# Kernel tuning notes

Hardware: AMD Instinct MI355X
Metric: run time of the kernel (lower is better)

## Reference

```python
import jax, jax.numpy as jnp
import numpy as np

L, B, D, N = 4096, 4, 1024, 16


def setup_inputs() -> dict:
    key = jax.random.key(0)
    ks = jax.random.split(key, 6)
    x = jax.random.normal(ks[0], (L, B, D), dtype=jnp.float32)
    delta = 0.2 * jax.random.normal(ks[1], (D, N, 1), dtype=jnp.float32)
    alpha = 0.2 * jax.random.normal(ks[2], (D, N, 1), dtype=jnp.float32)
    # beta init: N(0, 0.02) + 1.0 (val is all ones since i % 1 == 0 always)
    beta = 0.02 * jax.random.normal(ks[3], (D, N, 1), dtype=jnp.float32) + 1.0
    gamma = jax.random.normal(ks[4], (D, N), dtype=jnp.float32)
    omega = jax.random.normal(ks[5], (D,), dtype=jnp.float32)
    return {"x": x, "delta": delta, "alpha": alpha, "beta": beta,
            "gamma": gamma, "omega": omega}


def reference(x, delta, alpha, beta, gamma, omega):
    seq_len = x.shape[0]
    scale = (1.0 / gamma.shape[1]) ** 0.5
    # EMA coefficients
    p = jax.nn.sigmoid(delta)                      # (D, N, 1)
    q = 1.0 - p * jax.nn.sigmoid(alpha)            # (D, N, 1)
    # Vandermonde kernel: k[d, l] = sum_n p*beta * q^l * gamma*scale
    t = jnp.arange(seq_len, dtype=x.dtype)         # (L,)
    vander = t[None, None, :] * jnp.log(q)         # (D, N, L)
    kernel = p * beta * jnp.exp(vander)            # (D, N, L)
    k = jnp.einsum('dnl,dn->dl', kernel, gamma * scale)  # (D, L)
    # Residual path
    residual = x * omega                           # (L, B, D)
    # FFT causal convolution along time
    xt = jnp.transpose(x, (1, 2, 0))               # (B, D, L)
    n_fft = 2 * seq_len
    k_f = jnp.fft.rfft(k.astype(jnp.float32), n=n_fft)      # (D, n_fft//2+1)
    x_f = jnp.fft.rfft(xt.astype(jnp.float32), n=n_fft)     # (B, D, n_fft//2+1)
    out = jnp.fft.irfft(x_f * k_f, n=n_fft)[..., :seq_len]  # (B, D, L)
    out = out.astype(x.dtype)
    out = jax.nn.silu(jnp.transpose(out, (2, 0, 1)) + residual)  # (L, B, D)
    return out
```

## Files before the change

### kernel.cpp

```cpp
#include <hip/hip_runtime.h>
#include <hip/hip_cooperative_groups.h>
#include <math.h>

namespace cg = cooperative_groups;

#define D_SZ 1024
#define N_MODES 16
#define CH 4096
#define ROW 4096
#define C_CHUNKS 64
#define LC 64

__device__ __forceinline__ void load16(const float* __restrict__ p, int d, float v[16]) {
    const float4* p4 = (const float4*)(p + (size_t)d * 16);
#pragma unroll
    for (int r = 0; r < 4; ++r) {
        float4 t = p4[r];
        v[4*r+0] = t.x; v[4*r+1] = t.y; v[4*r+2] = t.z; v[4*r+3] = t.w;
    }
}

__device__ __forceinline__ void compute_qw(const float* __restrict__ delta,
                                           const float* __restrict__ alpha,
                                           const float* __restrict__ beta,
                                           const float* __restrict__ gamma,
                                           int d, float q[16], float w[16]) {
    float dl[16], al[16], bt[16], gm[16];
    load16(delta, d, dl); load16(alpha, d, al);
    load16(beta, d, bt);  load16(gamma, d, gm);
#pragma unroll
    for (int n = 0; n < 16; ++n) {
        float p  = 1.0f / (1.0f + __expf(-dl[n]));
        float sa = 1.0f / (1.0f + __expf(-al[n]));
        q[n] = 1.0f - p * sa;
        w[n] = p * bt[n] * gm[n] * 0.25f;
    }
}

__device__ __forceinline__ void phase1_body(const float* __restrict__ x, float* __restrict__ S,
    const float* __restrict__ delta, const float* __restrict__ alpha,
    const float* __restrict__ beta, const float* __restrict__ gamma, int j, int c) {
    int d = c & (D_SZ - 1);
    float q[16], w[16];
    compute_qw(delta, alpha, beta, gamma, d, q, w);
    float h[16];
#pragma unroll
    for (int n = 0; n < 16; ++n) h[n] = 0.0f;
    const float* xp = x + (size_t)j * (LC * ROW) + c;
#pragma unroll 2
    for (int s0 = 0; s0 < LC; s0 += 8) {
        float xv[8];
#pragma unroll
        for (int u = 0; u < 8; ++u) xv[u] = xp[(size_t)(s0 + u) * ROW];
#pragma unroll
        for (int u = 0; u < 8; ++u)
#pragma unroll
            for (int n = 0; n < 16; ++n) h[n] = fmaf(q[n], h[n], xv[u]);
    }
    float4* Sp = (float4*)(S + ((size_t)j * CH + c) * 16);
#pragma unroll
    for (int r = 0; r < 4; ++r)
        Sp[r] = make_float4(h[4*r], h[4*r+1], h[4*r+2], h[4*r+3]);
}

__device__ __forceinline__ void phase2_body(float* __restrict__ S,
    const float* __restrict__ delta, const float* __restrict__ alpha, int c2, int lane) {
    int d = c2 & (D_SZ - 1);
    float dl[16], al[16];
    load16(delta, d, dl); load16(alpha, d, al);
    float pw[16];
#pragma unroll
    for (int n = 0; n < 16; ++n) {
        float p  = 1.0f / (1.0f + __expf(-dl[n]));
        float sa = 1.0f / (1.0f + __expf(-al[n]));
        float qn = 1.0f - p * sa;
#pragma unroll
        for (int t = 0; t < 6; ++t) qn *= qn;
        pw[n] = qn;
    }
    float hh[16];
    float4* Sp = (float4*)(S + ((size_t)lane * CH + c2) * 16);
#pragma unroll
    for (int r = 0; r < 4; ++r) {
        float4 t = Sp[r];
        hh[4*r] = t.x; hh[4*r+1] = t.y; hh[4*r+2] = t.z; hh[4*r+3] = t.w;
    }
#pragma unroll
    for (int k = 1; k <= 32; k <<= 1) {
        float prev[16];
#pragma unroll
        for (int n = 0; n < 16; ++n) prev[n] = __shfl_up(hh[n], (unsigned)k, 64);
#pragma unroll
        for (int n = 0; n < 16; ++n) hh[n] = (lane >= k) ? fmaf(pw[n], prev[n], hh[n]) : hh[n];
#pragma unroll
        for (int n = 0; n < 16; ++n) pw[n] *= pw[n];
    }
    float cin[16];
#pragma unroll
    for (int n = 0; n < 16; ++n) {
        float t = __shfl_up(hh[n], 1u, 64);
        cin[n] = (lane == 0) ? 0.0f : t;
    }
#pragma unroll
    for (int r = 0; r < 4; ++r)
        Sp[r] = make_float4(cin[4*r], cin[4*r+1], cin[4*r+2], cin[4*r+3]);
}

__device__ __forceinline__ void phase3_body(const float* __restrict__ x,
    const float* __restrict__ S, float* __restrict__ out,
    const float* __restrict__ delta, const float* __restrict__ alpha,
    const float* __restrict__ beta, const float* __restrict__ gamma,
    const float* __restrict__ omega, int j, int c) {
    int d = c & (D_SZ - 1);
    float q[16], w[16];
    compute_qw(delta, alpha, beta, gamma, d, q, w);
    float om = omega[d];
    float h[16];
    const float4* Sp = (const float4*)(S + ((size_t)j * CH + c) * 16);
#pragma unroll
    for (int r = 0; r < 4; ++r) {
        float4 t = Sp[r];
        h[4*r] = t.x; h[4*r+1] = t.y; h[4*r+2] = t.z; h[4*r+3] = t.w;
    }
    size_t base = (size_t)j * (LC * ROW) + c;
#pragma unroll 2
    for (int s0 = 0; s0 < LC; s0 += 8) {
        float xv[8];
#pragma unroll
        for (int u = 0; u < 8; ++u) xv[u] = x[base + (size_t)(s0 + u) * ROW];
#pragma unroll
        for (int u = 0; u < 8; ++u) {
            float xu = xv[u];
            float y0 = 0.0f, y1 = 0.0f, y2 = 0.0f, y3 = 0.0f;
#pragma unroll
            for (int n = 0; n < 16; n += 4) {
                h[n]   = fmaf(q[n],   h[n],   xu); y0 = fmaf(w[n],   h[n],   y0);
                h[n+1] = fmaf(q[n+1], h[n+1], xu); y1 = fmaf(w[n+1], h[n+1], y1);
                h[n+2] = fmaf(q[n+2], h[n+2], xu); y2 = fmaf(w[n+2], h[n+2], y2);
                h[n+3] = fmaf(q[n+3], h[n+3], xu); y3 = fmaf(w[n+3], h[n+3], y3);
            }
            float z = (y0 + y1) + (y2 + y3) + xu * om;
            float r = z / (1.0f + __expf(-z));
            __builtin_nontemporal_store(r, &out[base + (size_t)(s0 + u) * ROW]);
        }
    }
}

__global__ __launch_bounds__(256, 4) void ema_fused(
    const float* __restrict__ x, const float* __restrict__ delta,
    const float* __restrict__ alpha, const float* __restrict__ beta,
    const float* __restrict__ gamma, const float* __restrict__ omega,
    float* __restrict__ S, float* __restrict__ out) {
    int tid = threadIdx.x;
    int j = blockIdx.x;
    int c = blockIdx.y * 256 + tid;
    phase1_body(x, S, delta, alpha, beta, gamma, j, c);
    cg::this_grid().sync();
    int gb = blockIdx.y * gridDim.x + blockIdx.x;
    phase2_body(S, delta, alpha, gb * 4 + (tid >> 6), tid & 63);
    cg::this_grid().sync();
    phase3_body(x, S, out, delta, alpha, beta, gamma, omega, j, c);
}

__global__ __launch_bounds__(256) void k_phase1(const float* __restrict__ x, float* __restrict__ S,
    const float* __restrict__ delta, const float* __restrict__ alpha,
    const float* __restrict__ beta, const float* __restrict__ gamma) {
    phase1_body(x, S, delta, alpha, beta, gamma, blockIdx.x, blockIdx.y * 256 + threadIdx.x);
}
__global__ __launch_bounds__(256) void k_phase2(float* __restrict__ S,
    const float* __restrict__ delta, const float* __restrict__ alpha) {
    phase2_body(S, delta, alpha, blockIdx.x * 4 + (threadIdx.x >> 6), threadIdx.x & 63);
}
__global__ __launch_bounds__(256) void k_phase3(const float* __restrict__ x,
    const float* __restrict__ S, float* __restrict__ out,
    const float* __restrict__ delta, const float* __restrict__ alpha,
    const float* __restrict__ beta, const float* __restrict__ gamma,
    const float* __restrict__ omega) {
    phase3_body(x, S, out, delta, alpha, beta, gamma, omega,
                blockIdx.x, blockIdx.y * 256 + threadIdx.x);
}

extern "C" void kernel_launch(void* const* d_in, const int* in_sizes, int n_in,
                              void* d_out, int out_size, void* d_ws, size_t ws_size,
                              hipStream_t stream) {
    const float* x     = (const float*)d_in[0];
    const float* delta = (const float*)d_in[1];
    const float* alpha = (const float*)d_in[2];
    const float* beta  = (const float*)d_in[3];
    const float* gamma = (const float*)d_in[4];
    const float* omega = (const float*)d_in[5];
    float* out = (float*)d_out;
    float* S   = (float*)d_ws;

    dim3 grid(C_CHUNKS, CH / 256);

    int maxBlocks = 0;
    hipError_t e = hipOccupancyMaxActiveBlocksPerMultiprocessor(
        &maxBlocks, (const void*)ema_fused, 256, 0);
    if (e == hipSuccess && maxBlocks >= 4) {
        void* args[] = {(void*)&x, (void*)&delta, (void*)&alpha, (void*)&beta,
                        (void*)&gamma, (void*)&omega, (void*)&S, (void*)&out};
        hipLaunchCooperativeKernel((const void*)ema_fused, grid, dim3(256, 1, 1),
                                   args, 0, stream);
    } else {
        k_phase1<<<grid, 256, 0, stream>>>(x, S, delta, alpha, beta, gamma);
        k_phase2<<<CH / 4, 256, 0, stream>>>(S, delta, alpha);
        k_phase3<<<grid, 256, 0, stream>>>(x, S, out, delta, alpha, beta, gamma, omega);
    }
}
```

Before: 164.5 us.

## Double-buffer x tiles through LDS with float4 loads in scan phases

Phases 1 and 3 now stage x through shared memory in 16-row sub-tiles using float4 global loads, double-buffered so the next sub-tile's loads are issued while the current one is consumed from LDS. This aims to replace scalar strided loads with wider coalesced loads and to hide global memory latency behind the recurrence FMAs. The cost is 32 KB of LDS per block plus extra __syncthreads, which may lower occupancy and break the cooperative-launch requirement of 4 blocks per CU, causing a fallback to the three-kernel path.

```diff
diff --git a/kernel.cpp b/kernel.cpp
--- a/kernel.cpp
+++ b/kernel.cpp
@@ -5,11 +5,13 @@
 namespace cg = cooperative_groups;
 
 #define D_SZ 1024
-#define N_MODES 16
 #define CH 4096
 #define ROW 4096
 #define C_CHUNKS 64
 #define LC 64
+#define SUB 16
+#define NSUB (LC / SUB)
+#define TILE_F (SUB * 256)
 
 __device__ __forceinline__ void load16(const float* __restrict__ p, int d, float v[16]) {
     const float4* p4 = (const float4*)(p + (size_t)d * 16);
@@ -37,30 +39,53 @@
     }
 }
 
+__device__ __forceinline__ void stage_issue(const float* __restrict__ x,
+                                            size_t rowBase, int tid, float4 r[4]) {
+    const float* p = x + rowBase + (size_t)(tid >> 6) * ROW + ((tid & 63) << 2);
+#pragma unroll
+    for (int k = 0; k < 4; ++k)
+        r[k] = *(const float4*)(p + (size_t)(4 * k) * ROW);
+}
+
+__device__ __forceinline__ void stage_commit(float* __restrict__ buf, int tid,
+                                             const float4 r[4]) {
+#pragma unroll
+    for (int k = 0; k < 4; ++k)
+        *(float4*)(buf + ((tid >> 6) + 4 * k) * 256 + ((tid & 63) << 2)) = r[k];
+}
+
 __device__ __forceinline__ void phase1_body(const float* __restrict__ x, float* __restrict__ S,
     const float* __restrict__ delta, const float* __restrict__ alpha,
-    const float* __restrict__ beta, const float* __restrict__ gamma, int j, int c) {
+    const float* __restrict__ beta, const float* __restrict__ gamma,
+    int j, int cgrp, int tid, float* __restrict__ lds) {
+    int c = cgrp * 256 + tid;
     int d = c & (D_SZ - 1);
     float q[16], w[16];
     compute_qw(delta, alpha, beta, gamma, d, q, w);
     float h[16];
 #pragma unroll
     for (int n = 0; n < 16; ++n) h[n] = 0.0f;
-    const float* xp = x + (size_t)j * (LC * ROW) + c;
-#pragma unroll 2
-    for (int s0 = 0; s0 < LC; s0 += 8) {
-        float xv[8];
-#pragma unroll
-        for (int u = 0; u < 8; ++u) xv[u] = xp[(size_t)(s0 + u) * ROW];
-#pragma unroll
-        for (int u = 0; u < 8; ++u)
-#pragma unroll
-            for (int n = 0; n < 16; ++n) h[n] = fmaf(q[n], h[n], xv[u]);
+
+    size_t rb = (size_t)(j * LC) * ROW + (size_t)cgrp * 256;
+    float4 r[4];
+    stage_issue(x, rb, tid, r);
+    stage_commit(lds, tid, r);
+    for (int st = 0; st < NSUB; ++st) {
+        if (st + 1 < NSUB) stage_issue(x, rb + (size_t)((st + 1) * SUB) * ROW, tid, r);
+        __syncthreads();
+        const float* cb = lds + (st & 1) * TILE_F;
+#pragma unroll
+        for (int l = 0; l < SUB; ++l) {
+            float xu = cb[l * 256 + tid];
+#pragma unroll
+            for (int n = 0; n < 16; ++n) h[n] = fmaf(q[n], h[n], xu);
+        }
+        if (st + 1 < NSUB) stage_commit(lds + ((st + 1) & 1) * TILE_F, tid, r);
     }
     float4* Sp = (float4*)(S + ((size_t)j * CH + c) * 16);
 #pragma unroll
-    for (int r = 0; r < 4; ++r)
-        Sp[r] = make_float4(h[4*r], h[4*r+1], h[4*r+2], h[4*r+3]);
+    for (int rr = 0; rr < 4; ++rr)
+        Sp[rr] = make_float4(h[4*rr], h[4*rr+1], h[4*rr+2], h[4*rr+3]);
 }
 
 __device__ __forceinline__ void phase2_body(float* __restrict__ S,
@@ -81,9 +106,9 @@
     float hh[16];
     float4* Sp = (float4*)(S + ((size_t)lane * CH + c2) * 16);
 #pragma unroll
-    for (int r = 0; r < 4; ++r) {
-        float4 t = Sp[r];
-        hh[4*r] = t.x; hh[4*r+1] = t.y; hh[4*r+2] = t.z; hh[4*r+3] = t.w;
+    for (int rr = 0; rr < 4; ++rr) {
+        float4 t = Sp[rr];
+        hh[4*rr] = t.x; hh[4*rr+1] = t.y; hh[4*rr+2] = t.z; hh[4*rr+3] = t.w;
     }
 #pragma unroll
     for (int k = 1; k <= 32; k <<= 1) {
@@ -102,15 +127,16 @@
         cin[n] = (lane == 0) ? 0.0f : t;
     }
 #pragma unroll
-    for (int r = 0; r < 4; ++r)
-        Sp[r] = make_float4(cin[4*r], cin[4*r+1], cin[4*r+2], cin[4*r+3]);
+    for (int rr = 0; rr < 4; ++rr)
+        Sp[rr] = make_float4(cin[4*rr], cin[4*rr+1], cin[4*rr+2], cin[4*rr+3]);
 }
 
 __device__ __forceinline__ void phase3_body(const float* __restrict__ x,
     const float* __restrict__ S, float* __restrict__ out,
     const float* __restrict__ delta, const float* __restrict__ alpha,
     const float* __restrict__ beta, const float* __restrict__ gamma,
-    const float* __restrict__ omega, int j, int c) {
+    const float* __restrict__ omega, int j, int cgrp, int tid, float* __restrict__ lds) {
+    int c = cgrp * 256 + tid;
     int d = c & (D_SZ - 1);
     float q[16], w[16];
     compute_qw(delta, alpha, beta, gamma, d, q, w);
@@ -118,19 +144,23 @@
     float h[16];
     const float4* Sp = (const float4*)(S + ((size_t)j * CH + c) * 16);
 #pragma unroll
-    for (int r = 0; r < 4; ++r) {
-        float4 t = Sp[r];
-        h[4*r] = t.x; h[4*r+1] = t.y; h[4*r+2] = t.z; h[4*r+3] = t.w;
-    }
-    size_t base = (size_t)j * (LC * ROW) + c;
-#pragma unroll 2
-    for (int s0 = 0; s0 < LC; s0 += 8) {
-        float xv[8];
-#pragma unroll
-        for (int u = 0; u < 8; ++u) xv[u] = x[base + (size_t)(s0 + u) * ROW];
-#pragma unroll
-        for (int u = 0; u < 8; ++u) {
-            float xu = xv[u];
+    for (int rr = 0; rr < 4; ++rr) {
+        float4 t = Sp[rr];
+        h[4*rr] = t.x; h[4*rr+1] = t.y; h[4*rr+2] = t.z; h[4*rr+3] = t.w;
+    }
+
+    size_t rb = (size_t)(j * LC) * ROW + (size_t)cgrp * 256;
+    float4 r[4];
+    stage_issue(x, rb, tid, r);
+    stage_commit(lds, tid, r);
+    for (int st = 0; st < NSUB; ++st) {
+        if (st + 1 < NSUB) stage_issue(x, rb + (size_t)((st + 1) * SUB) * ROW, tid, r);
+        __syncthreads();
+        const float* cb = lds + (st & 1) * TILE_F;
+        size_t obase = rb + (size_t)(st * SUB) * ROW + (size_t)tid;
+#pragma unroll
+        for (int l = 0; l < SUB; ++l) {
+            float xu = cb[l * 256 + tid];
             float y0 = 0.0f, y1 = 0.0f, y2 = 0.0f, y3 = 0.0f;
 #pragma unroll
             for (int n = 0; n < 16; n += 4) {
@@ -140,9 +170,10 @@
                 h[n+3] = fmaf(q[n+3], h[n+3], xu); y3 = fmaf(w[n+3], h[n+3], y3);
             }
             float z = (y0 + y1) + (y2 + y3) + xu * om;
-            float r = z / (1.0f + __expf(-z));
-            __builtin_nontemporal_store(r, &out[base + (size_t)(s0 + u) * ROW]);
+            float res = z / (1.0f + __expf(-z));
+            __builtin_nontemporal_store(res, &out[obase + (size_t)l * ROW]);
         }
+        if (st + 1 < NSUB) stage_commit(lds + ((st + 1) & 1) * TILE_F, tid, r);
     }
 }
 
@@ -151,21 +182,23 @@
     const float* __restrict__ alpha, const float* __restrict__ beta,
     const float* __restrict__ gamma, const float* __restrict__ omega,
     float* __restrict__ S, float* __restrict__ out) {
+    __shared__ float lds[2 * TILE_F];
     int tid = threadIdx.x;
     int j = blockIdx.x;
-    int c = blockIdx.y * 256 + tid;
-    phase1_body(x, S, delta, alpha, beta, gamma, j, c);
+    int cgrp = blockIdx.y;
+    phase1_body(x, S, delta, alpha, beta, gamma, j, cgrp, tid, lds);
     cg::this_grid().sync();
-    int gb = blockIdx.y * gridDim.x + blockIdx.x;
+    int gb = cgrp * gridDim.x + j;
     phase2_body(S, delta, alpha, gb * 4 + (tid >> 6), tid & 63);
     cg::this_grid().sync();
-    phase3_body(x, S, out, delta, alpha, beta, gamma, omega, j, c);
+    phase3_body(x, S, out, delta, alpha, beta, gamma, omega, j, cgrp, tid, lds);
 }
 
 __global__ __launch_bounds__(256) void k_phase1(const float* __restrict__ x, float* __restrict__ S,
     const float* __restrict__ delta, const float* __restrict__ alpha,
     const float* __restrict__ beta, const float* __restrict__ gamma) {
-    phase1_body(x, S, delta, alpha, beta, gamma, blockIdx.x, blockIdx.y * 256 + threadIdx.x);
+    __shared__ float lds[2 * TILE_F];
+    phase1_body(x, S, delta, alpha, beta, gamma, blockIdx.x, blockIdx.y, threadIdx.x, lds);
 }
 __global__ __launch_bounds__(256) void k_phase2(float* __restrict__ S,
     const float* __restrict__ delta, const float* __restrict__ alpha) {
@@ -176,8 +209,9 @@
     const float* __restrict__ delta, const float* __restrict__ alpha,
     const float* __restrict__ beta, const float* __restrict__ gamma,
     const float* __restrict__ omega) {
+    __shared__ float lds[2 * TILE_F];
     phase3_body(x, S, out, delta, alpha, beta, gamma, omega,
-                blockIdx.x, blockIdx.y * 256 + threadIdx.x);
+                blockIdx.x, blockIdx.y, threadIdx.x, lds);
 }
 
 extern "C" void kernel_launch(void* const* d_in, const int* in_sizes, int n_in,
```

Measured after the change: 191.5 us. 1.16x slower.

## Replace cooperative fused kernel with three launches using 128 smaller chunks

Applied to the files above, without the earlier changes.

Drops the cooperative-groups fused kernel with grid syncs and always runs three separate kernels. The chunk count doubles to 128 with 32 timesteps each, and phase 2 handles two chunks per lane: it combines pairs serially before the 64-lane shuffle scan, then expands the result back. Phases 1 and 3 use explicit double-buffered register loads of x. Non-temporal output stores are removed. This trades grid-sync cost and the occupancy limit of the cooperative launch for extra launch overhead and doubled S workspace traffic.

```diff
diff --git a/kernel.cpp b/kernel.cpp
--- a/kernel.cpp
+++ b/kernel.cpp
@@ -1,15 +1,12 @@
 #include <hip/hip_runtime.h>
-#include <hip/hip_cooperative_groups.h>
 #include <math.h>
 
-namespace cg = cooperative_groups;
-
 #define D_SZ 1024
-#define N_MODES 16
 #define CH 4096
 #define ROW 4096
-#define C_CHUNKS 64
-#define LC 64
+#define C_CHUNKS 128
+#define LC 32
+#define SQ_LC 5
 
 __device__ __forceinline__ void load16(const float* __restrict__ p, int d, float v[16]) {
     const float4* p4 = (const float4*)(p + (size_t)d * 16);
@@ -37,54 +34,77 @@
     }
 }
 
-__device__ __forceinline__ void phase1_body(const float* __restrict__ x, float* __restrict__ S,
+__device__ __forceinline__ void loadg(const float* __restrict__ xp, int g, float v[8]) {
+#pragma unroll
+    for (int u = 0; u < 8; ++u) v[u] = xp[(size_t)(g * 8 + u) * ROW];
+}
+
+__device__ __forceinline__ void compg(float h[16], const float q[16], const float v[8]) {
+#pragma unroll
+    for (int u = 0; u < 8; ++u) {
+        float xu = v[u];
+#pragma unroll
+        for (int n = 0; n < 16; ++n) h[n] = fmaf(q[n], h[n], xu);
+    }
+}
+
+__global__ __launch_bounds__(256) void k_phase1(const float* __restrict__ x,
+    float* __restrict__ S,
     const float* __restrict__ delta, const float* __restrict__ alpha,
-    const float* __restrict__ beta, const float* __restrict__ gamma, int j, int c) {
+    const float* __restrict__ beta, const float* __restrict__ gamma) {
+    int tid = threadIdx.x;
+    int j = blockIdx.x;
+    int c = blockIdx.y * 256 + tid;
     int d = c & (D_SZ - 1);
     float q[16], w[16];
     compute_qw(delta, alpha, beta, gamma, d, q, w);
     float h[16];
 #pragma unroll
     for (int n = 0; n < 16; ++n) h[n] = 0.0f;
-    const float* xp = x + (size_t)j * (LC * ROW) + c;
-#pragma unroll 2
-    for (int s0 = 0; s0 < LC; s0 += 8) {
-        float xv[8];
-#pragma unroll
-        for (int u = 0; u < 8; ++u) xv[u] = xp[(size_t)(s0 + u) * ROW];
-#pragma unroll
-        for (int u = 0; u < 8; ++u)
-#pragma unroll
-            for (int n = 0; n < 16; ++n) h[n] = fmaf(q[n], h[n], xv[u]);
-    }
+    const float* xp = x + (size_t)j * LC * ROW + c;
+    float xa[8], xb[8];
+    loadg(xp, 0, xa);
+    loadg(xp, 1, xb); compg(h, q, xa);
+    loadg(xp, 2, xa); compg(h, q, xb);
+    loadg(xp, 3, xb); compg(h, q, xa);
+    compg(h, q, xb);
     float4* Sp = (float4*)(S + ((size_t)j * CH + c) * 16);
 #pragma unroll
     for (int r = 0; r < 4; ++r)
         Sp[r] = make_float4(h[4*r], h[4*r+1], h[4*r+2], h[4*r+3]);
 }
 
-__device__ __forceinline__ void phase2_body(float* __restrict__ S,
-    const float* __restrict__ delta, const float* __restrict__ alpha, int c2, int lane) {
-    int d = c2 & (D_SZ - 1);
+__global__ __launch_bounds__(256) void k_phase2(float* __restrict__ S,
+    const float* __restrict__ delta, const float* __restrict__ alpha) {
+    int lane = threadIdx.x & 63;
+    int wv   = threadIdx.x >> 6;
+    int c    = blockIdx.x * 4 + wv;
+    int d    = c & (D_SZ - 1);
     float dl[16], al[16];
     load16(delta, d, dl); load16(alpha, d, al);
-    float pw[16];
+    float A[16], pw[16];
 #pragma unroll
     for (int n = 0; n < 16; ++n) {
         float p  = 1.0f / (1.0f + __expf(-dl[n]));
         float sa = 1.0f / (1.0f + __expf(-al[n]));
         float qn = 1.0f - p * sa;
 #pragma unroll
-        for (int t = 0; t < 6; ++t) qn *= qn;
-        pw[n] = qn;
+        for (int t = 0; t < SQ_LC; ++t) qn *= qn;
+        A[n]  = qn;
+        pw[n] = qn * qn;
+    }
+    float4* Spa = (float4*)(S + ((size_t)(2 * lane)     * CH + c) * 16);
+    float4* Spb = (float4*)(S + ((size_t)(2 * lane + 1) * CH + c) * 16);
+    float sa16[16], sb16[16];
+#pragma unroll
+    for (int r = 0; r < 4; ++r) {
+        float4 ta = Spa[r], tb = Spb[r];
+        sa16[4*r] = ta.x; sa16[4*r+1] = ta.y; sa16[4*r+2] = ta.z; sa16[4*r+3] = ta.w;
+        sb16[4*r] = tb.x; sb16[4*r+1] = tb.y; sb16[4*r+2] = tb.z; sb16[4*r+3] = tb.w;
     }
     float hh[16];
-    float4* Sp = (float4*)(S + ((size_t)lane * CH + c2) * 16);
 #pragma unroll
-    for (int r = 0; r < 4; ++r) {
-        float4 t = Sp[r];
-        hh[4*r] = t.x; hh[4*r+1] = t.y; hh[4*r+2] = t.z; hh[4*r+3] = t.w;
-    }
+    for (int n = 0; n < 16; ++n) hh[n] = fmaf(A[n], sa16[n], sb16[n]);
 #pragma unroll
     for (int k = 1; k <= 32; k <<= 1) {
         float prev[16];
@@ -95,22 +115,49 @@
 #pragma unroll
         for (int n = 0; n < 16; ++n) pw[n] *= pw[n];
     }
-    float cin[16];
+    float Hb[16];
 #pragma unroll
     for (int n = 0; n < 16; ++n) {
         float t = __shfl_up(hh[n], 1u, 64);
-        cin[n] = (lane == 0) ? 0.0f : t;
+        Hb[n] = (lane == 0) ? 0.0f : t;
     }
 #pragma unroll
-    for (int r = 0; r < 4; ++r)
-        Sp[r] = make_float4(cin[4*r], cin[4*r+1], cin[4*r+2], cin[4*r+3]);
+    for (int r = 0; r < 4; ++r) {
+        Spa[r] = make_float4(Hb[4*r], Hb[4*r+1], Hb[4*r+2], Hb[4*r+3]);
+        Spb[r] = make_float4(fmaf(A[4*r],   Hb[4*r],   sa16[4*r]),
+                             fmaf(A[4*r+1], Hb[4*r+1], sa16[4*r+1]),
+                             fmaf(A[4*r+2], Hb[4*r+2], sa16[4*r+2]),
+                             fmaf(A[4*r+3], Hb[4*r+3], sa16[4*r+3]));
+    }
 }
 
-__device__ __forceinline__ void phase3_body(const float* __restrict__ x,
+__device__ __forceinline__ void comp_store(float h[16], const float q[16], const float w[16],
+                                           float om, const float v[8],
+                                           float* __restrict__ outp, int g) {
+#pragma unroll
+    for (int u = 0; u < 8; ++u) {
+        float xu = v[u];
+        float y0 = 0.0f, y1 = 0.0f, y2 = 0.0f, y3 = 0.0f;
+#pragma unroll
+        for (int n = 0; n < 16; n += 4) {
+            h[n]   = fmaf(q[n],   h[n],   xu); y0 = fmaf(w[n],   h[n],   y0);
+            h[n+1] = fmaf(q[n+1], h[n+1], xu); y1 = fmaf(w[n+1], h[n+1], y1);
+            h[n+2] = fmaf(q[n+2], h[n+2], xu); y2 = fmaf(w[n+2], h[n+2], y2);
+            h[n+3] = fmaf(q[n+3], h[n+3], xu); y3 = fmaf(w[n+3], h[n+3], y3);
+        }
+        float z = (y0 + y1) + (y2 + y3) + xu * om;
+        outp[(size_t)(g * 8 + u) * ROW] = z / (1.0f + __expf(-z));
+    }
+}
+
+__global__ __launch_bounds__(256) void k_phase3(const float* __restrict__ x,
     const float* __restrict__ S, float* __restrict__ out,
     const float* __restrict__ delta, const float* __restrict__ alpha,
     const float* __restrict__ beta, const float* __restrict__ gamma,
-    const float* __restrict__ omega, int j, int c) {
+    const float* __restrict__ omega) {
+    int tid = threadIdx.x;
+    int j = blockIdx.x;
+    int c = blockIdx.y * 256 + tid;
     int d = c & (D_SZ - 1);
     float q[16], w[16];
     compute_qw(delta, alpha, beta, gamma, d, q, w);
@@ -122,62 +169,14 @@
         float4 t = Sp[r];
         h[4*r] = t.x; h[4*r+1] = t.y; h[4*r+2] = t.z; h[4*r+3] = t.w;
     }
-    size_t base = (size_t)j * (LC * ROW) + c;
-#pragma unroll 2
-    for (int s0 = 0; s0 < LC; s0 += 8) {
-        float xv[8];
-#pragma unroll
-        for (int u = 0; u < 8; ++u) xv[u] = x[base + (size_t)(s0 + u) * ROW];
-#pragma unroll
-        for (int u = 0; u < 8; ++u) {
-            float xu = xv[u];
-            float y0 = 0.0f, y1 = 0.0f, y2 = 0.0f, y3 = 0.0f;
-#pragma unroll
-            for (int n = 0; n < 16; n += 4) {
-                h[n]   = fmaf(q[n],   h[n],   xu); y0 = fmaf(w[n],   h[n],   y0);
-                h[n+1] = fmaf(q[n+1], h[n+1], xu); y1 = fmaf(w[n+1], h[n+1], y1);
-                h[n+2] = fmaf(q[n+2], h[n+2], xu); y2 = fmaf(w[n+2], h[n+2], y2);
-                h[n+3] = fmaf(q[n+3], h[n+3], xu); y3 = fmaf(w[n+3], h[n+3], y3);
-            }
-            float z = (y0 + y1) + (y2 + y3) + xu * om;
-            float r = z / (1.0f + __expf(-z));
-            __builtin_nontemporal_store(r, &out[base + (size_t)(s0 + u) * ROW]);
-        }
-    }
-}
-
-__global__ __launch_bounds__(256, 4) void ema_fused(
-    const float* __restrict__ x, const float* __restrict__ delta,
-    const float* __restrict__ alpha, const float* __restrict__ beta,
-    const float* __restrict__ gamma, const float* __restrict__ omega,
-    float* __restrict__ S, float* __restrict__ out) {
-    int tid = threadIdx.x;
-    int j = blockIdx.x;
-    int c = blockIdx.y * 256 + tid;
-    phase1_body(x, S, delta, alpha, beta, gamma, j, c);
-    cg::this_grid().sync();
-    int gb = blockIdx.y * gridDim.x + blockIdx.x;
-    phase2_body(S, delta, alpha, gb * 4 + (tid >> 6), tid & 63);
-    cg::this_grid().sync();
-    phase3_body(x, S, out, delta, alpha, beta, gamma, omega, j, c);
-}
-
-__global__ __launch_bounds__(256) void k_phase1(const float* __restrict__ x, float* __restrict__ S,
-    const float* __restrict__ delta, const float* __restrict__ alpha,
-    const float* __restrict__ beta, const float* __restrict__ gamma) {
-    phase1_body(x, S, delta, alpha, beta, gamma, blockIdx.x, blockIdx.y * 256 + threadIdx.x);
-}
-__global__ __launch_bounds__(256) void k_phase2(float* __restrict__ S,
-    const float* __restrict__ delta, const float* __restrict__ alpha) {
-    phase2_body(S, delta, alpha, blockIdx.x * 4 + (threadIdx.x >> 6), threadIdx.x & 63);
-}
-__global__ __launch_bounds__(256) void k_phase3(const float* __restrict__ x,
-    const float* __restrict__ S, float* __restrict__ out,
-    const float* __restrict__ delta, const float* __restrict__ alpha,
-    const float* __restrict__ beta, const float* __restrict__ gamma,
-    const float* __restrict__ omega) {
-    phase3_body(x, S, out, delta, alpha, beta, gamma, omega,
-                blockIdx.x, blockIdx.y * 256 + threadIdx.x);
+    const float* xp = x + (size_t)j * LC * ROW + c;
+    float* outp = out + (size_t)j * LC * ROW + c;
+    float xa[8], xb[8];
+    loadg(xp, 0, xa);
+    loadg(xp, 1, xb); comp_store(h, q, w, om, xa, outp, 0);
+    loadg(xp, 2, xa); comp_store(h, q, w, om, xb, outp, 1);
+    loadg(xp, 3, xb); comp_store(h, q, w, om, xa, outp, 2);
+    comp_store(h, q, w, om, xb, outp, 3);
 }
 
 extern "C" void kernel_launch(void* const* d_in, const int* in_sizes, int n_in,
@@ -192,19 +191,8 @@
     float* out = (float*)d_out;
     float* S   = (float*)d_ws;
 
-    dim3 grid(C_CHUNKS, CH / 256);
-
-    int maxBlocks = 0;
-    hipError_t e = hipOccupancyMaxActiveBlocksPerMultiprocessor(
-        &maxBlocks, (const void*)ema_fused, 256, 0);
-    if (e == hipSuccess && maxBlocks >= 4) {
-        void* args[] = {(void*)&x, (void*)&delta, (void*)&alpha, (void*)&beta,
-                        (void*)&gamma, (void*)&omega, (void*)&S, (void*)&out};
-        hipLaunchCooperativeKernel((const void*)ema_fused, grid, dim3(256, 1, 1),
-                                   args, 0, stream);
-    } else {
-        k_phase1<<<grid, 256, 0, stream>>>(x, S, delta, alpha, beta, gamma);
-        k_phase2<<<CH / 4, 256, 0, stream>>>(S, delta, alpha);
-        k_phase3<<<grid, 256, 0, stream>>>(x, S, out, delta, alpha, beta, gamma, omega);
-    }
+    dim3 grid13(C_CHUNKS, CH / 256);
+    k_phase1<<<grid13, 256, 0, stream>>>(x, S, delta, alpha, beta, gamma);
+    k_phase2<<<CH / 4, 256, 0, stream>>>(S, delta, alpha);
+    k_phase3<<<grid13, 256, 0, stream>>>(x, S, out, delta, alpha, beta, gamma, omega);
 }
```

After: 197.6 us. 1.2x slower.
